# Kernel optimization log

Measured on AMD Instinct MI355X. Metric: run time of the kernel, lower is better.

Reference implementation:

```python
import jax, jax.numpy as jnp
import numpy as np

# Model dims (from init_kwargs + mamba_ssm defaults)
D_MODEL = 1024
N_LAYER = 2
D_STATE = 16
D_CONV = 4
D_INNER = 2 * D_MODEL          # expand=2
DT_RANK = D_MODEL // 16        # 64
VOCAB = 32000
BATCH, SEQLEN = 2, 1024


def setup_inputs() -> dict:
    key = jax.random.key(0)
    ks = jax.random.split(key, 10)
    s = 0.02
    x = jax.random.randint(ks[0], (BATCH, SEQLEN), 0, VOCAB)
    embedding = jax.random.normal(ks[1], (VOCAB, D_MODEL), dtype=jnp.float32) * s
    norm_w = jnp.ones((N_LAYER, D_MODEL), dtype=jnp.float32)
    in_proj_w = jax.random.normal(ks[2], (N_LAYER, 2 * D_INNER, D_MODEL), dtype=jnp.float32) * s
    conv_w = jax.random.normal(ks[3], (N_LAYER, D_INNER, D_CONV), dtype=jnp.float32) * (1.0 / np.sqrt(D_CONV))
    conv_b = jnp.zeros((N_LAYER, D_INNER), dtype=jnp.float32)
    x_proj_w = jax.random.normal(ks[4], (N_LAYER, DT_RANK + 2 * D_STATE, D_INNER), dtype=jnp.float32) * s
    dt_proj_w = jax.random.normal(ks[5], (N_LAYER, D_INNER, DT_RANK), dtype=jnp.float32) * (DT_RANK ** -0.5)
    # inverse-softplus of dt_init ~ 0.01 (mamba default dt range)
    dt_bias = jnp.full((N_LAYER, D_INNER), float(np.log(np.expm1(0.01))), dtype=jnp.float32)
    A_log = jnp.log(jnp.broadcast_to(jnp.arange(1, D_STATE + 1, dtype=jnp.float32), (N_LAYER, D_INNER, D_STATE)))
    D = jnp.ones((N_LAYER, D_INNER), dtype=jnp.float32)
    out_proj_w = jax.random.normal(ks[6], (N_LAYER, D_MODEL, D_INNER), dtype=jnp.float32) * s
    final_norm_w = jnp.ones((D_MODEL,), dtype=jnp.float32)
    return {"x": x, "embedding": embedding, "norm_w": norm_w, "in_proj_w": in_proj_w,
            "conv_w": conv_w, "conv_b": conv_b, "x_proj_w": x_proj_w, "dt_proj_w": dt_proj_w,
            "dt_bias": dt_bias, "A_log": A_log, "D": D, "out_proj_w": out_proj_w,
            "final_norm_w": final_norm_w}


def _rmsnorm(h, w, eps=1e-5):
    return h * jax.lax.rsqrt(jnp.mean(h * h, axis=-1, keepdims=True) + eps) * w


def _scan_combine(c1, c2):
    a1, b1 = c1
    a2, b2 = c2
    return a2 * a1, a2 * b1 + b2


def _mamba_block(h, norm_w, in_proj_w, conv_w, conv_b, x_proj_w, dt_proj_w, dt_bias, A_log, D, out_proj_w):
    u = _rmsnorm(h, norm_w)
    xz = jnp.einsum('bld,ed->ble', u, in_proj_w)           # [B,L,2*D_INNER]
    xi, z = jnp.split(xz, 2, axis=-1)
    # depthwise causal conv1d, kernel D_CONV
    k = conv_w.T[:, None, :]                               # [D_CONV, 1, D_INNER]
    xc = jax.lax.conv_general_dilated(xi, k, (1,), [(D_CONV - 1, 0)],
                                      dimension_numbers=('NLC', 'LIO', 'NLC'),
                                      feature_group_count=D_INNER) + conv_b
    xc = jax.nn.silu(xc)
    dbl = jnp.einsum('bld,ed->ble', xc, x_proj_w)          # [B,L,DT_RANK+2*D_STATE]
    dt_low = dbl[..., :DT_RANK]
    Bm = dbl[..., DT_RANK:DT_RANK + D_STATE]
    Cm = dbl[..., DT_RANK + D_STATE:]
    dt = jax.nn.softplus(jnp.einsum('blr,dr->bld', dt_low, dt_proj_w) + dt_bias)
    A = -jnp.exp(A_log)                                    # [D_INNER, D_STATE]
    a = jnp.exp(dt[..., None] * A)                         # [B,L,D_INNER,D_STATE]
    b = dt[..., None] * Bm[:, :, None, :] * xc[..., None]  # [B,L,D_INNER,D_STATE]
    hs = jax.lax.associative_scan(_scan_combine, (a, b), axis=1)[1]
    y = jnp.einsum('bldn,bln->bld', hs, Cm) + xc * D
    y = y * jax.nn.silu(z)
    return h + jnp.einsum('bld,md->blm', y, out_proj_w)


def reference(x, embedding, norm_w, in_proj_w, conv_w, conv_b, x_proj_w, dt_proj_w,
              dt_bias, A_log, D, out_proj_w, final_norm_w):
    h = embedding[x]                                       # [B,L,D_MODEL]
    for i in range(N_LAYER):
        h = _mamba_block(h, norm_w[i], in_proj_w[i], conv_w[i], conv_b[i], x_proj_w[i],
                         dt_proj_w[i], dt_bias[i], A_log[i], D[i], out_proj_w[i])
    h = _rmsnorm(h, final_norm_w)
    logits = jnp.einsum('bld,vd->blv', h, embedding)       # tied lm head
    return logits
```

## Files before the change

kernel.cpp:

```cpp
#include <hip/hip_runtime.h>
#include <hip/hip_bf16.h>
#include <math.h>

#define D_MODEL 1024
#define N_LAYER 2
#define D_STATE 16
#define D_CONV  4
#define D_INNER 2048
#define DT_RANK 64
#define VOCAB   32000
#define BATCH   2
#define SEQLEN  1024
#define TOKENS  (BATCH*SEQLEN)
#define NC      32
#define CL      32

typedef __hip_bfloat16 bf16;
typedef __bf16 bf16x8 __attribute__((ext_vector_type(8)));
typedef float f32x4 __attribute__((ext_vector_type(4)));

__device__ inline void gld_lds16(const bf16* g, bf16* l) {
    __builtin_amdgcn_global_load_lds(
        (const __attribute__((address_space(1))) void*)g,
        (__attribute__((address_space(3))) void*)l, 16, 0, 0);
}

__device__ inline float softplus_fast(float v) {
    return (v > 20.f) ? v : __logf(1.f + __expf(v));
}
__device__ inline float silu_fast(float v) {
    return v / (1.f + __expf(-v));
}
__device__ inline float bfu(unsigned short s) {
    unsigned u = ((unsigned)s) << 16;
    float f;
    __builtin_memcpy(&f, &u, 4);
    return f;
}

__global__ __launch_bounds__(256) void embed_rms(const int* __restrict__ x,
                                                 const float* __restrict__ emb,
                                                 const float* __restrict__ w,
                                                 float* __restrict__ h,
                                                 bf16* __restrict__ u) {
    int t = blockIdx.x;
    int tok = x[t];
    float4 v = ((const float4*)(emb + (size_t)tok * D_MODEL))[threadIdx.x];
    ((float4*)(h + (size_t)t * D_MODEL))[threadIdx.x] = v;
    float ss = v.x*v.x + v.y*v.y + v.z*v.z + v.w*v.w;
    #pragma unroll
    for (int off = 32; off > 0; off >>= 1) ss += __shfl_down(ss, off);
    __shared__ float red[4];
    int lane = threadIdx.x & 63, wid = threadIdx.x >> 6;
    if (lane == 0) red[wid] = ss;
    __syncthreads();
    float tot = red[0] + red[1] + red[2] + red[3];
    float scale = rsqrtf(tot * (1.0f / (float)D_MODEL) + 1e-5f);
    float4 wq = ((const float4*)w)[threadIdx.x];
    size_t o = (size_t)t * D_MODEL + threadIdx.x * 4;
    u[o+0] = __float2bfloat16(v.x * scale * wq.x);
    u[o+1] = __float2bfloat16(v.y * scale * wq.y);
    u[o+2] = __float2bfloat16(v.z * scale * wq.z);
    u[o+3] = __float2bfloat16(v.w * scale * wq.w);
}

__global__ __launch_bounds__(256) void f32_to_bf16(const float* __restrict__ s,
                                                   bf16* __restrict__ d, int n) {
    int i = (blockIdx.x * 256 + threadIdx.x) * 4;
    if (i < n) {
        float4 v = *(const float4*)(s + i);
        d[i+0] = __float2bfloat16(v.x);
        d[i+1] = __float2bfloat16(v.y);
        d[i+2] = __float2bfloat16(v.z);
        d[i+3] = __float2bfloat16(v.w);
    }
}

__global__ __launch_bounds__(256) void conv_xproj_pad(const float* __restrict__ s,
                                                      bf16* __restrict__ d) {
    int col = blockIdx.x * 256 + threadIdx.x;
    int row = blockIdx.y;
    int layer = blockIdx.z;
    float v = (row < 96) ? s[((size_t)layer * 96 + row) * D_INNER + col] : 0.f;
    d[((size_t)layer * 128 + row) * D_INNER + col] = __float2bfloat16(v);
}

__global__ __launch_bounds__(256) void gemm_bf16(
    const bf16* __restrict__ A, int lda,
    const bf16* __restrict__ W, int ldw,
    float* __restrict__ C, int ldc,
    int N, int K, int acc, int swz, int M, int bfout)
{
    __shared__ bf16 lds[2][2][128 * 64];
    int bx = blockIdx.x, by = blockIdx.y;
    if (swz) {
        int bid = by * gridDim.x + bx;
        int q = (gridDim.x * gridDim.y) >> 3;
        int n = (bid & 7) * q + (bid >> 3);
        by = n % gridDim.y;
        bx = n / gridDim.y;
    }
    const int z = blockIdx.z;
    A += (size_t)z * K;
    W += (size_t)z * K;
    float* Cf = C + (size_t)z * M * (size_t)ldc;
    bf16*  Cb = (bf16*)C + (size_t)z * M * (size_t)ldc;

    const int tid  = threadIdx.x;
    const int wave = tid >> 6;
    const int lane = tid & 63;
    const int wr = wave >> 1, wc = wave & 1;
    const size_t rowBase = (size_t)by * 128;
    const size_t colBase = (size_t)bx * 128;

    const int srow = 8 * wave + (lane >> 3);
    const int scol = ((lane & 7) ^ (lane >> 3)) << 3;
    const bf16* aGs = A + (rowBase + srow) * (size_t)lda + scol;
    const bf16* bGs = W + (colBase + srow) * (size_t)ldw + scol;

#define STAGE(tt, bb) do {                                                      \
        const size_t kofs_ = (size_t)(tt) * 64;                                 \
        _Pragma("unroll")                                                       \
        for (int i_ = 0; i_ < 4; ++i_) {                                        \
            gld_lds16(aGs + kofs_ + (size_t)(32 * i_) * lda,                    \
                      &lds[bb][0][(32 * i_ + 8 * wave) * 64]);                  \
            gld_lds16(bGs + kofs_ + (size_t)(32 * i_) * ldw,                    \
                      &lds[bb][1][(32 * i_ + 8 * wave) * 64]);                  \
        }                                                                       \
    } while (0)

    f32x4 accv[4][4];
    #pragma unroll
    for (int i = 0; i < 4; ++i)
        #pragma unroll
        for (int j = 0; j < 4; ++j)
            accv[i][j] = f32x4{0.f, 0.f, 0.f, 0.f};

    const int arow0 = wr * 64 + (lane & 15);
    const int brow0 = wc * 64 + (lane & 15);
    const int h8  = (lane >> 4) << 3;
    const int sw8 = (lane & 7) << 3;

    const int NT = K >> 6;
    STAGE(0, 0);
    for (int t = 0; t < NT; ++t) {
        const int cur = t & 1;
        if (t + 1 < NT) {
            STAGE(t + 1, cur ^ 1);
            asm volatile("s_waitcnt vmcnt(8)" ::: "memory");
        } else {
            asm volatile("s_waitcnt vmcnt(0)" ::: "memory");
        }
        __builtin_amdgcn_s_barrier();

        const bf16* Ab = &lds[cur][0][0];
        const bf16* Bb = &lds[cur][1][0];
        #pragma unroll
        for (int kk = 0; kk < 2; ++kk) {
            const int cs = ((kk << 5) + h8) ^ sw8;
            bf16x8 af[4], bv[4];
            #pragma unroll
            for (int i = 0; i < 4; ++i)
                af[i] = *(const bf16x8*)(Ab + (arow0 + 16 * i) * 64 + cs);
            #pragma unroll
            for (int j = 0; j < 4; ++j)
                bv[j] = *(const bf16x8*)(Bb + (brow0 + 16 * j) * 64 + cs);
            #pragma unroll
            for (int i = 0; i < 4; ++i)
                #pragma unroll
                for (int j = 0; j < 4; ++j)
                    accv[i][j] = __builtin_amdgcn_mfma_f32_16x16x32_bf16(
                        af[i], bv[j], accv[i][j], 0, 0, 0);
        }
        asm volatile("s_waitcnt lgkmcnt(0)" ::: "memory");
        __builtin_amdgcn_s_barrier();
    }
#undef STAGE

    const int cl = lane & 15;
    const int rg = (lane >> 4) * 4;
    #pragma unroll
    for (int i = 0; i < 4; ++i) {
        #pragma unroll
        for (int j = 0; j < 4; ++j) {
            int col = (int)colBase + wc * 64 + j * 16 + cl;
            if (col < N) {
                size_t base = (rowBase + wr * 64 + i * 16 + rg) * (size_t)ldc + col;
                if (bfout) {
                    #pragma unroll
                    for (int r = 0; r < 4; ++r)
                        Cb[base + (size_t)r * ldc] = __float2bfloat16(accv[i][j][r]);
                } else {
                    #pragma unroll
                    for (int r = 0; r < 4; ++r) {
                        size_t idx = base + (size_t)r * ldc;
                        Cf[idx] = acc ? Cf[idx] + accv[i][j][r] : accv[i][j][r];
                    }
                }
            }
        }
    }
}

__global__ __launch_bounds__(512) void gemm_wide3(
    const bf16* __restrict__ A,
    const bf16* __restrict__ W,
    float* __restrict__ C, int ldc, int bfout)
{
    __shared__ bf16 ldsA[3][256 * 32];
    __shared__ bf16 ldsB[3][128 * 32];
    int bx = blockIdx.x, by = blockIdx.y;
    {
        int bid = by * gridDim.x + bx;
        int n = (bid & 7) * ((gridDim.x * gridDim.y) >> 3) + (bid >> 3);
        by = n & 7;
        bx = n >> 3;
    }
    const int tid  = threadIdx.x;
    const int wave = tid >> 6;
    const int lane = tid & 63;
    const int wr = wave >> 1;
    const int wc = wave & 1;
    const size_t rowBase = (size_t)by * 256;
    const size_t colBase = (size_t)bx * 128;

    const int srow   = lane >> 2;
    const int schunk = ((lane & 3) ^ ((lane >> 3) & 3)) << 3;
    const bf16* aG0 = A + (rowBase + 16 * wave       + srow) * (size_t)D_MODEL + schunk;
    const bf16* aG1 = A + (rowBase + 128 + 16 * wave + srow) * (size_t)D_MODEL + schunk;
    const bf16* bG  = W + (colBase + 16 * wave       + srow) * (size_t)D_MODEL + schunk;

#define STAGEW(tt, sAp, sBp) do {                                               \
        const size_t ko_ = (size_t)(tt) * 32;                                   \
        gld_lds16(aG0 + ko_, (sAp) + 512 * wave);                               \
        gld_lds16(aG1 + ko_, (sAp) + 512 * (8 + wave));                         \
        gld_lds16(bG  + ko_, (sBp) + 512 * wave);                               \
    } while (0)

    f32x4 accv[4][4];
    #pragma unroll
    for (int i = 0; i < 4; ++i)
        #pragma unroll
        for (int j = 0; j < 4; ++j)
            accv[i][j] = f32x4{0.f, 0.f, 0.f, 0.f};

    const int l15 = lane & 15;
    const int cs = (((lane >> 4) ^ ((l15 >> 1) & 3)) << 3);
    const int arow0 = wr * 64 + l15;
    const int brow0 = wc * 64 + l15;

    STAGEW(0, &ldsA[0][0], &ldsB[0][0]);
    STAGEW(1, &ldsA[1][0], &ldsB[1][0]);

    int rs = 0, ps = 2;
    #pragma unroll 1
    for (int t = 0; t < 32; ++t) {
        if (t < 31) { asm volatile("s_waitcnt vmcnt(3)" ::: "memory"); }
        else        { asm volatile("s_waitcnt vmcnt(0)" ::: "memory"); }
        __builtin_amdgcn_s_barrier();
        __builtin_amdgcn_sched_barrier(0);

        if (t + 2 < 32) STAGEW(t + 2, &ldsA[ps][0], &ldsB[ps][0]);

        const bf16* Ab = &ldsA[rs][0];
        const bf16* Bb = &ldsB[rs][0];
        bf16x8 af[4], bv[4];
        #pragma unroll
        for (int i = 0; i < 4; ++i)
            af[i] = *(const bf16x8*)(Ab + (arow0 + 16 * i) * 32 + cs);
        #pragma unroll
        for (int j = 0; j < 4; ++j)
            bv[j] = *(const bf16x8*)(Bb + (brow0 + 16 * j) * 32 + cs);
        #pragma unroll
        for (int i = 0; i < 4; ++i)
            #pragma unroll
            for (int j = 0; j < 4; ++j)
                accv[i][j] = __builtin_amdgcn_mfma_f32_16x16x32_bf16(
                    af[i], bv[j], accv[i][j], 0, 0, 0);

        rs = (rs == 2) ? 0 : rs + 1;
        ps = (ps == 2) ? 0 : ps + 1;
    }
#undef STAGEW

    const int cl = l15;
    const int rg = (lane >> 4) * 4;
    #pragma unroll
    for (int i = 0; i < 4; ++i) {
        #pragma unroll
        for (int j = 0; j < 4; ++j) {
            int col = (int)colBase + wc * 64 + j * 16 + cl;
            size_t base = (rowBase + wr * 64 + i * 16 + rg) * (size_t)ldc + col;
            if (bfout) {
                bf16* Cb = (bf16*)C;
                #pragma unroll
                for (int r = 0; r < 4; ++r)
                    Cb[base + (size_t)r * ldc] = __float2bfloat16(accv[i][j][r]);
            } else {
                #pragma unroll
                for (int r = 0; r < 4; ++r)
                    C[base + (size_t)r * ldc] = accv[i][j][r];
            }
        }
    }
}

__global__ __launch_bounds__(256) void conv_silu_kernel(const bf16* __restrict__ xz,
                                                        const float* __restrict__ cw,
                                                        const float* __restrict__ cb,
                                                        bf16* __restrict__ xcb) {
    int d = blockIdx.x * 256 + threadIdx.x;
    int l0 = blockIdx.y * 8;
    int b = blockIdx.z;
    float w0 = cw[d*4+0], w1 = cw[d*4+1], w2 = cw[d*4+2], w3 = cw[d*4+3];
    float bias = cb[d];
    float win0 = (l0 >= 3) ? __bfloat162float(xz[((size_t)b * SEQLEN + l0 - 3) * (2*D_INNER) + d]) : 0.f;
    float win1 = (l0 >= 2) ? __bfloat162float(xz[((size_t)b * SEQLEN + l0 - 2) * (2*D_INNER) + d]) : 0.f;
    float win2 = (l0 >= 1) ? __bfloat162float(xz[((size_t)b * SEQLEN + l0 - 1) * (2*D_INNER) + d]) : 0.f;
    #pragma unroll
    for (int i = 0; i < 8; ++i) {
        float cur = __bfloat162float(xz[((size_t)b * SEQLEN + l0 + i) * (2*D_INNER) + d]);
        float acc = bias + w0*win0 + w1*win1 + w2*win2 + w3*cur;
        float s = silu_fast(acc);
        xcb[((size_t)b * SEQLEN + l0 + i) * D_INNER + d] = __float2bfloat16(s);
        win0 = win1; win1 = win2; win2 = cur;
    }
}

__global__ __launch_bounds__(256) void reduce_xproj(const float* __restrict__ px,
                                                    float* __restrict__ dblf,
                                                    bf16* __restrict__ dbl_b) {
    int i = blockIdx.x * 256 + threadIdx.x;
    float s = 0.f;
    #pragma unroll
    for (int z = 0; z < 8; ++z) s += px[(size_t)z * (TOKENS*96) + i];
    dblf[i] = s;
    dbl_b[i] = __float2bfloat16(s);
}

__global__ __launch_bounds__(256) void reduce_oproj_rms(const bf16* __restrict__ po,
                                                        float* __restrict__ h,
                                                        const float* __restrict__ w,
                                                        bf16* __restrict__ u) {
    int t = blockIdx.x;
    size_t base = (size_t)t * D_MODEL + threadIdx.x * 4;
    ushort4 ua = *(const ushort4*)(po + base);
    ushort4 ub = *(const ushort4*)(po + (size_t)TOKENS * D_MODEL + base);
    float4 hv = *(const float4*)(h + base);
    hv.x += bfu(ua.x) + bfu(ub.x);
    hv.y += bfu(ua.y) + bfu(ub.y);
    hv.z += bfu(ua.z) + bfu(ub.z);
    hv.w += bfu(ua.w) + bfu(ub.w);
    *(float4*)(h + base) = hv;
    float ss = hv.x*hv.x + hv.y*hv.y + hv.z*hv.z + hv.w*hv.w;
    #pragma unroll
    for (int off = 32; off > 0; off >>= 1) ss += __shfl_down(ss, off);
    __shared__ float red[4];
    int lane = threadIdx.x & 63, wid = threadIdx.x >> 6;
    if (lane == 0) red[wid] = ss;
    __syncthreads();
    float tot = red[0] + red[1] + red[2] + red[3];
    float scale = rsqrtf(tot * (1.0f / (float)D_MODEL) + 1e-5f);
    float4 wq = ((const float4*)w)[threadIdx.x];
    u[base+0] = __float2bfloat16(hv.x * scale * wq.x);
    u[base+1] = __float2bfloat16(hv.y * scale * wq.y);
    u[base+2] = __float2bfloat16(hv.z * scale * wq.z);
    u[base+3] = __float2bfloat16(hv.w * scale * wq.w);
}

__global__ __launch_bounds__(256) void scan_chunk(const bf16* __restrict__ dtp,
                                                  const float* __restrict__ dt_bias,
                                                  const float* __restrict__ dbl,
                                                  const bf16* __restrict__ xc,
                                                  const float* __restrict__ A_log,
                                                  float* __restrict__ dts_out,
                                                  float* __restrict__ sfin) {
    int d = blockIdx.x * 256 + threadIdx.x;
    int c = blockIdx.y;
    int b = blockIdx.z;
    __shared__ float Bs[CL][D_STATE];
    for (int i = threadIdx.x; i < CL * D_STATE; i += 256) {
        int l = i >> 4, n = i & 15;
        Bs[l][n] = dbl[((size_t)b * SEQLEN + c * CL + l) * 96 + DT_RANK + n];
    }
    __syncthreads();
    float A[D_STATE];
    #pragma unroll
    for (int n = 0; n < D_STATE; ++n) A[n] = -__expf(A_log[d * D_STATE + n]);
    float bias = dt_bias[d];
    float st[D_STATE];
    #pragma unroll
    for (int n = 0; n < D_STATE; ++n) st[n] = 0.f;
    float dts = 0.f;
    for (int l = 0; l < CL; ++l) {
        size_t t = (size_t)b * SEQLEN + c * CL + l;
        float dtv = softplus_fast(__bfloat162float(dtp[t * D_INNER + d]) + bias);
        dts += dtv;
        float dx = dtv * __bfloat162float(xc[t * D_INNER + d]);
        #pragma unroll
        for (int n = 0; n < D_STATE; ++n) {
            float a = __expf(dtv * A[n]);
            st[n] = a * st[n] + dx * Bs[l][n];
        }
    }
    dts_out[((size_t)b * NC + c) * D_INNER + d] = dts;
    #pragma unroll
    for (int n = 0; n < D_STATE; ++n) {
        size_t o = (((size_t)b * NC + c) * D_STATE + n) * D_INNER + d;
        sfin[o] = st[n];
    }
}

__global__ __launch_bounds__(256) void scan_carry(const float* __restrict__ dts,
                                                  const float* __restrict__ sfin,
                                                  const float* __restrict__ A_log,
                                                  float* __restrict__ initS) {
    int idx = blockIdx.x * 256 + threadIdx.x;
    int d = idx & (D_INNER - 1);
    int n = (idx >> 11) & (D_STATE - 1);
    int b = idx >> 15;
    float A = -__expf(A_log[d * D_STATE + n]);
    float st = 0.f;
    for (int c = 0; c < NC; ++c) {
        size_t o = (((size_t)b * NC + c) * D_STATE + n) * D_INNER + d;
        initS[o] = st;
        float ap = __expf(dts[((size_t)b * NC + c) * D_INNER + d] * A);
        st = ap * st + sfin[o];
    }
}

__global__ __launch_bounds__(256) void scan_emit(const bf16* __restrict__ dtp,
                                                 const float* __restrict__ dt_bias,
                                                 const float* __restrict__ dbl,
                                                 const bf16* __restrict__ xc,
                                                 const bf16* __restrict__ xz,
                                                 const float* __restrict__ A_log,
                                                 const float* __restrict__ Dp,
                                                 const float* __restrict__ initS,
                                                 bf16* __restrict__ y) {
    int d = blockIdx.x * 256 + threadIdx.x;
    int c = blockIdx.y;
    int b = blockIdx.z;
    __shared__ float BCs[CL][2 * D_STATE];
    for (int i = threadIdx.x; i < CL * 2 * D_STATE; i += 256) {
        int l = i >> 5, n = i & 31;
        BCs[l][n] = dbl[((size_t)b * SEQLEN + c * CL + l) * 96 + DT_RANK + n];
    }
    __syncthreads();
    float A[D_STATE];
    #pragma unroll
    for (int n = 0; n < D_STATE; ++n) A[n] = -__expf(A_log[d * D_STATE + n]);
    float bias = dt_bias[d];
    float Dv = Dp[d];
    float st[D_STATE];
    #pragma unroll
    for (int n = 0; n < D_STATE; ++n)
        st[n] = initS[(((size_t)b * NC + c) * D_STATE + n) * D_INNER + d];
    for (int l = 0; l < CL; ++l) {
        size_t t = (size_t)b * SEQLEN + c * CL + l;
        float dtv = softplus_fast(__bfloat162float(dtp[t * D_INNER + d]) + bias);
        float xcv = __bfloat162float(xc[t * D_INNER + d]);
        float dx = dtv * xcv;
        float acc = 0.f;
        #pragma unroll
        for (int n = 0; n < D_STATE; ++n) {
            float a = __expf(dtv * A[n]);
            st[n] = a * st[n] + dx * BCs[l][n];
            acc += st[n] * BCs[l][D_STATE + n];
        }
        acc += xcv * Dv;
        float zv = __bfloat162float(xz[t * (2 * D_INNER) + D_INNER + d]);
        y[t * D_INNER + d] = __float2bfloat16(acc * silu_fast(zv));
    }
}

extern "C" void kernel_launch(void* const* d_in, const int* in_sizes, int n_in,
                              void* d_out, int out_size, void* d_ws, size_t ws_size,
                              hipStream_t stream) {
    const int*   x          = (const int*)  d_in[0];
    const float* emb        = (const float*)d_in[1];
    const float* norm_w     = (const float*)d_in[2];
    const float* in_proj_w  = (const float*)d_in[3];
    const float* conv_w     = (const float*)d_in[4];
    const float* conv_b     = (const float*)d_in[5];
    const float* x_proj_w   = (const float*)d_in[6];
    const float* dt_proj_w  = (const float*)d_in[7];
    const float* dt_bias    = (const float*)d_in[8];
    const float* A_log      = (const float*)d_in[9];
    const float* Dp         = (const float*)d_in[10];
    const float* out_proj_w = (const float*)d_in[11];
    const float* fnorm_w    = (const float*)d_in[12];
    float* out = (float*)d_out;
    float* ws  = (float*)d_ws;

    bf16*  embf   = (bf16*)ws;
    bf16*  u_b    = (bf16*)(ws + 16384000);
    bf16*  xz_b   = (bf16*)(ws + 17432576);
    bf16*  dtp_b  = (bf16*)(ws + 25821184);
    bf16*  xc_b   = (bf16*)(ws + 30015488);
    float* h      = ws + 36306944;
    float* dblf   = ws + 38404096;
    bf16*  dbl_b  = (bf16*)(ws + 38600704);
    bf16*  y_b    = (bf16*)(ws + 38699008);
    bf16*  inpj_b = (bf16*)(ws + 40796160);
    bf16*  xpj_b  = (bf16*)(ws + 44990464);
    bf16*  dtpj_b = (bf16*)(ws + 45252608);
    bf16*  otpj_b = (bf16*)(ws + 45383680);
    float* dts    = ws + 47480832;
    float* sfin   = ws + 49577984;
    float* initS  = ws + 51675136;
    float* px     = ws + 53772288;
    bf16*  po_b   = (bf16*)(ws + 55345152);

    f32_to_bf16<<<(VOCAB*D_MODEL/4 + 255)/256, 256, 0, stream>>>(emb, embf, VOCAB*D_MODEL);
    f32_to_bf16<<<(2*2*D_INNER*D_MODEL/4 + 255)/256, 256, 0, stream>>>(in_proj_w,  inpj_b, 2*2*D_INNER*D_MODEL);
    conv_xproj_pad<<<dim3(D_INNER/256, 128, N_LAYER), 256, 0, stream>>>(x_proj_w, xpj_b);
    f32_to_bf16<<<(2*D_INNER*DT_RANK/4 + 255)/256, 256, 0, stream>>>(dt_proj_w,  dtpj_b, 2*D_INNER*DT_RANK);
    f32_to_bf16<<<(2*D_MODEL*D_INNER/4 + 255)/256, 256, 0, stream>>>(out_proj_w, otpj_b, 2*D_MODEL*D_INNER);

    embed_rms<<<TOKENS, 256, 0, stream>>>(x, emb, norm_w, h, u_b);

    for (int layer = 0; layer < N_LAYER; ++layer) {
        gemm_wide3<<<dim3(4096/128, TOKENS/256), 512, 0, stream>>>(
            u_b, inpj_b + (size_t)layer * 2 * D_INNER * D_MODEL,
            (float*)xz_b, 2 * D_INNER, 1);
        conv_silu_kernel<<<dim3(D_INNER/256, SEQLEN/8, BATCH), 256, 0, stream>>>(
            xz_b, conv_w + (size_t)layer * D_INNER * D_CONV, conv_b + layer * D_INNER,
            xc_b);
        gemm_bf16<<<dim3(1, TOKENS/128, 8), 256, 0, stream>>>(
            xc_b, D_INNER, xpj_b + (size_t)layer * 128 * D_INNER, D_INNER,
            px, 96, 96, 256, 0, 0, TOKENS, 0);
        reduce_xproj<<<(TOKENS*96)/256, 256, 0, stream>>>(px, dblf, dbl_b);
        gemm_bf16<<<dim3(D_INNER/128, TOKENS/128), 256, 0, stream>>>(
            dbl_b, 96, dtpj_b + (size_t)layer * D_INNER * DT_RANK, DT_RANK,
            (float*)dtp_b, D_INNER, D_INNER, DT_RANK, 0, 1, TOKENS, 1);
        scan_chunk<<<dim3(D_INNER/256, NC, BATCH), 256, 0, stream>>>(
            dtp_b, dt_bias + layer * D_INNER, dblf, xc_b,
            A_log + (size_t)layer * D_INNER * D_STATE, dts, sfin);
        scan_carry<<<(BATCH*D_STATE*D_INNER)/256, 256, 0, stream>>>(
            dts, sfin, A_log + (size_t)layer * D_INNER * D_STATE, initS);
        scan_emit<<<dim3(D_INNER/256, NC, BATCH), 256, 0, stream>>>(
            dtp_b, dt_bias + layer * D_INNER, dblf, xc_b, xz_b,
            A_log + (size_t)layer * D_INNER * D_STATE, Dp + layer * D_INNER,
            initS, y_b);
        gemm_bf16<<<dim3(D_MODEL/128, TOKENS/128, 2), 256, 0, stream>>>(
            y_b, D_INNER, otpj_b + (size_t)layer * D_MODEL * D_INNER, D_INNER,
            (float*)po_b, D_MODEL, D_MODEL, 1024, 0, 1, TOKENS, 1);
        reduce_oproj_rms<<<TOKENS, 256, 0, stream>>>(
            po_b, h, (layer + 1 < N_LAYER) ? (norm_w + (layer + 1) * D_MODEL) : fnorm_w,
            u_b);
    }

    gemm_wide3<<<dim3(VOCAB/128, TOKENS/256), 512, 0, stream>>>(u_b, embf, out, VOCAB, 0);
}
```

Before: 531.2 us.

## Halve scan chunk length, double x_proj split-K, store scan carries in bf16

Changes the chunked selective scan from 32 chunks of 32 steps to 64 chunks of 16 steps, which doubles the parallelism of the chunk and emit kernels and halves their serial length, at the cost of a longer carry pass. Doubles the split-K factor of the x_proj GEMM from 8 to 16 for more blocks. Drops the fp32 copy of dbl and stores inter-chunk states (sfin/initS) in bf16 to cut memory traffic, which loses precision in the scan carries.

```diff
diff --git a/kernel.cpp b/kernel.cpp
--- a/kernel.cpp
+++ b/kernel.cpp
@@ -12,8 +12,9 @@
 #define BATCH   2
 #define SEQLEN  1024
 #define TOKENS  (BATCH*SEQLEN)
-#define NC      32
-#define CL      32
+#define NC      64
+#define CL      16
+#define XPZ     16
 
 typedef __hip_bfloat16 bf16;
 typedef __bf16 bf16x8 __attribute__((ext_vector_type(8)));
@@ -328,13 +329,11 @@
 }
 
 __global__ __launch_bounds__(256) void reduce_xproj(const float* __restrict__ px,
-                                                    float* __restrict__ dblf,
                                                     bf16* __restrict__ dbl_b) {
     int i = blockIdx.x * 256 + threadIdx.x;
     float s = 0.f;
     #pragma unroll
-    for (int z = 0; z < 8; ++z) s += px[(size_t)z * (TOKENS*96) + i];
-    dblf[i] = s;
+    for (int z = 0; z < XPZ; ++z) s += px[(size_t)z * (TOKENS*96) + i];
     dbl_b[i] = __float2bfloat16(s);
 }
 
@@ -370,18 +369,19 @@
 
 __global__ __launch_bounds__(256) void scan_chunk(const bf16* __restrict__ dtp,
                                                   const float* __restrict__ dt_bias,
-                                                  const float* __restrict__ dbl,
+                                                  const bf16* __restrict__ dbl,
                                                   const bf16* __restrict__ xc,
                                                   const float* __restrict__ A_log,
                                                   float* __restrict__ dts_out,
-                                                  float* __restrict__ sfin) {
+                                                  bf16* __restrict__ sfin) {
     int d = blockIdx.x * 256 + threadIdx.x;
     int c = blockIdx.y;
     int b = blockIdx.z;
     __shared__ float Bs[CL][D_STATE];
-    for (int i = threadIdx.x; i < CL * D_STATE; i += 256) {
+    {
+        int i = threadIdx.x;
         int l = i >> 4, n = i & 15;
-        Bs[l][n] = dbl[((size_t)b * SEQLEN + c * CL + l) * 96 + DT_RANK + n];
+        Bs[l][n] = __bfloat162float(dbl[((size_t)b * SEQLEN + c * CL + l) * 96 + DT_RANK + n]);
     }
     __syncthreads();
     float A[D_STATE];
@@ -407,14 +407,14 @@
     #pragma unroll
     for (int n = 0; n < D_STATE; ++n) {
         size_t o = (((size_t)b * NC + c) * D_STATE + n) * D_INNER + d;
-        sfin[o] = st[n];
+        sfin[o] = __float2bfloat16(st[n]);
     }
 }
 
 __global__ __launch_bounds__(256) void scan_carry(const float* __restrict__ dts,
-                                                  const float* __restrict__ sfin,
+                                                  const bf16* __restrict__ sfin,
                                                   const float* __restrict__ A_log,
-                                                  float* __restrict__ initS) {
+                                                  bf16* __restrict__ initS) {
     int idx = blockIdx.x * 256 + threadIdx.x;
     int d = idx & (D_INNER - 1);
     int n = (idx >> 11) & (D_STATE - 1);
@@ -423,20 +423,20 @@
     float st = 0.f;
     for (int c = 0; c < NC; ++c) {
         size_t o = (((size_t)b * NC + c) * D_STATE + n) * D_INNER + d;
-        initS[o] = st;
+        initS[o] = __float2bfloat16(st);
         float ap = __expf(dts[((size_t)b * NC + c) * D_INNER + d] * A);
-        st = ap * st + sfin[o];
+        st = ap * st + __bfloat162float(sfin[o]);
     }
 }
 
 __global__ __launch_bounds__(256) void scan_emit(const bf16* __restrict__ dtp,
                                                  const float* __restrict__ dt_bias,
-                                                 const float* __restrict__ dbl,
+                                                 const bf16* __restrict__ dbl,
                                                  const bf16* __restrict__ xc,
                                                  const bf16* __restrict__ xz,
                                                  const float* __restrict__ A_log,
                                                  const float* __restrict__ Dp,
-                                                 const float* __restrict__ initS,
+                                                 const bf16* __restrict__ initS,
                                                  bf16* __restrict__ y) {
     int d = blockIdx.x * 256 + threadIdx.x;
     int c = blockIdx.y;
@@ -444,7 +444,7 @@
     __shared__ float BCs[CL][2 * D_STATE];
     for (int i = threadIdx.x; i < CL * 2 * D_STATE; i += 256) {
         int l = i >> 5, n = i & 31;
-        BCs[l][n] = dbl[((size_t)b * SEQLEN + c * CL + l) * 96 + DT_RANK + n];
+        BCs[l][n] = __bfloat162float(dbl[((size_t)b * SEQLEN + c * CL + l) * 96 + DT_RANK + n]);
     }
     __syncthreads();
     float A[D_STATE];
@@ -455,7 +455,7 @@
     float st[D_STATE];
     #pragma unroll
     for (int n = 0; n < D_STATE; ++n)
-        st[n] = initS[(((size_t)b * NC + c) * D_STATE + n) * D_INNER + d];
+        st[n] = __bfloat162float(initS[(((size_t)b * NC + c) * D_STATE + n) * D_INNER + d]);
     for (int l = 0; l < CL; ++l) {
         size_t t = (size_t)b * SEQLEN + c * CL + l;
         float dtv = softplus_fast(__bfloat162float(dtp[t * D_INNER + d]) + bias);
@@ -499,7 +499,6 @@
     bf16*  dtp_b  = (bf16*)(ws + 25821184);
     bf16*  xc_b   = (bf16*)(ws + 30015488);
     float* h      = ws + 36306944;
-    float* dblf   = ws + 38404096;
     bf16*  dbl_b  = (bf16*)(ws + 38600704);
     bf16*  y_b    = (bf16*)(ws + 38699008);
     bf16*  inpj_b = (bf16*)(ws + 40796160);
@@ -507,10 +506,10 @@
     bf16*  dtpj_b = (bf16*)(ws + 45252608);
     bf16*  otpj_b = (bf16*)(ws + 45383680);
     float* dts    = ws + 47480832;
-    float* sfin   = ws + 49577984;
-    float* initS  = ws + 51675136;
+    bf16*  sfin   = (bf16*)(ws + 49577984);
+    bf16*  initS  = (bf16*)(ws + 51675136);
     float* px     = ws + 53772288;
-    bf16*  po_b   = (bf16*)(ws + 55345152);
+    bf16*  po_b   = (bf16*)(ws + 56918016);
 
     f32_to_bf16<<<(VOCAB*D_MODEL/4 + 255)/256, 256, 0, stream>>>(emb, embf, VOCAB*D_MODEL);
     f32_to_bf16<<<(2*2*D_INNER*D_MODEL/4 + 255)/256, 256, 0, stream>>>(in_proj_w,  inpj_b, 2*2*D_INNER*D_MODEL);
@@ -527,20 +526,20 @@
         conv_silu_kernel<<<dim3(D_INNER/256, SEQLEN/8, BATCH), 256, 0, stream>>>(
             xz_b, conv_w + (size_t)layer * D_INNER * D_CONV, conv_b + layer * D_INNER,
             xc_b);
-        gemm_bf16<<<dim3(1, TOKENS/128, 8), 256, 0, stream>>>(
+        gemm_bf16<<<dim3(1, TOKENS/128, XPZ), 256, 0, stream>>>(
             xc_b, D_INNER, xpj_b + (size_t)layer * 128 * D_INNER, D_INNER,
-            px, 96, 96, 256, 0, 0, TOKENS, 0);
-        reduce_xproj<<<(TOKENS*96)/256, 256, 0, stream>>>(px, dblf, dbl_b);
+            px, 96, 96, 128, 0, 0, TOKENS, 0);
+        reduce_xproj<<<(TOKENS*96)/256, 256, 0, stream>>>(px, dbl_b);
         gemm_bf16<<<dim3(D_INNER/128, TOKENS/128), 256, 0, stream>>>(
             dbl_b, 96, dtpj_b + (size_t)layer * D_INNER * DT_RANK, DT_RANK,
             (float*)dtp_b, D_INNER, D_INNER, DT_RANK, 0, 1, TOKENS, 1);
         scan_chunk<<<dim3(D_INNER/256, NC, BATCH), 256, 0, stream>>>(
-            dtp_b, dt_bias + layer * D_INNER, dblf, xc_b,
+            dtp_b, dt_bias + layer * D_INNER, dbl_b, xc_b,
             A_log + (size_t)layer * D_INNER * D_STATE, dts, sfin);
         scan_carry<<<(BATCH*D_STATE*D_INNER)/256, 256, 0, stream>>>(
             dts, sfin, A_log + (size_t)layer * D_INNER * D_STATE, initS);
         scan_emit<<<dim3(D_INNER/256, NC, BATCH), 256, 0, stream>>>(
-            dtp_b, dt_bias + layer * D_INNER, dblf, xc_b, xz_b,
+            dtp_b, dt_bias + layer * D_INNER, dbl_b, xc_b, xz_b,
             A_log + (size_t)layer * D_INNER * D_STATE, Dp + layer * D_INNER,
             initS, y_b);
         gemm_bf16<<<dim3(D_MODEL/128, TOKENS/128, 2), 256, 0, stream>>>(
```

Result: faster. 512.6 us (median of 2 runs) (-3.5%).
